# Kernel tuning notes

Hardware: AMD Instinct MI355X
Metric: run time of the kernel (lower is better)

Reference implementation:

```python
import jax, jax.numpy as jnp
import numpy as np
import itertools


def setup_inputs() -> dict:
    key = jax.random.key(0)
    k1, k2 = jax.random.split(key)
    vol = jax.random.normal(k1, (2, 160, 192, 224, 2), dtype=jnp.float32)
    trf = jax.random.normal(k2, (2, 160, 192, 224, 3), dtype=jnp.float32)
    return {"vol": vol, "trf": trf}


def _interpn_linear(vol, loc):
    """N-D multilinear interpolation of vol [*shape, C] at float locations.

    loc: list of ndims arrays, each [*shape], giving absolute sample coords.
    Out-of-domain points are clamped to the boundary (fill_value=None).
    Matches neurite's interpn('linear') math.
    """
    shape = vol.shape[:-1]
    ndims = len(shape)
    C = vol.shape[-1]
    maxs = [s - 1 for s in shape]

    # clip sample locations into the valid domain
    loc = [jnp.clip(l, 0.0, float(m)) for l, m in zip(loc, maxs)]
    loc0 = [jnp.clip(jnp.floor(l), 0.0, float(m)) for l, m in zip(loc, maxs)]
    loc1 = [jnp.clip(l0 + 1.0, 0.0, float(m)) for l0, m in zip(loc0, maxs)]
    # corner-0 weight is (loc1 - loc), corner-1 weight is its complement
    w_c0 = [l1 - l for l1, l in zip(loc1, loc)]
    w_c1 = [1.0 - w for w in w_c0]

    idx0 = [l.astype(jnp.int32) for l in loc0]
    idx1 = [l.astype(jnp.int32) for l in loc1]

    # row-major strides for flat gather
    strides = np.concatenate([np.cumprod(np.array(shape[::-1]))[::-1][1:], [1]]).astype(np.int32)
    vol_flat = vol.reshape(-1, C)

    out = jnp.zeros(shape + (C,), dtype=vol.dtype)
    for corner in itertools.product((0, 1), repeat=ndims):
        flat_idx = 0
        wt = 1.0
        for d in range(ndims):
            i = idx0[d] if corner[d] == 0 else idx1[d]
            w = w_c0[d] if corner[d] == 0 else w_c1[d]
            flat_idx = flat_idx + i * int(strides[d])
            wt = wt * w
        gathered = jnp.take(vol_flat, flat_idx, axis=0)  # [*shape, C]
        out = out + wt[..., None] * gathered
    return out


def reference(vol, trf):
    # single_transform=True: only the first batch element is used
    v = vol[0]   # [D1, D2, D3, C]
    t = trf[0]   # [D1, D2, D3, 3] dense shift (ij indexing)
    shape = v.shape[:-1]
    ndims = len(shape)
    # absolute sample locations = meshgrid + shift
    loc = []
    for d in range(ndims):
        ax = [1] * ndims
        ax[d] = shape[d]
        grid_d = jnp.arange(shape[d], dtype=t.dtype).reshape(ax)
        loc.append(grid_d + t[..., d])
    return _interpn_linear(v, loc)
```

## Files before the change

### kernel.cpp

```cpp
#include <hip/hip_runtime.h>


constexpr int D0 = 160, D1 = 192, D2 = 224;
constexpr int GT_K = D2 / 16;
constexpr int GT_J = D1 / 8;
constexpr int GT_I = D0 / 4;
constexpr int NBLOCKS = GT_K * GT_J * GT_I;

typedef float float4u __attribute__((ext_vector_type(4), aligned(8)));

__device__ __forceinline__ float2 sample_one(const float2* __restrict__ vol2,
                                             int i, int j, int k,
                                             float s0, float s1, float s2)
{
    float l0 = fminf(fmaxf((float)i + s0, 0.0f), (float)(D0 - 1));
    float l1 = fminf(fmaxf((float)j + s1, 0.0f), (float)(D1 - 1));
    float l2 = fminf(fmaxf((float)k + s2, 0.0f), (float)(D2 - 1));

    float f0 = floorf(l0), f1 = floorf(l1), f2 = floorf(l2);
    float g0 = fminf(f0 + 1.0f, (float)(D0 - 1));
    float g1 = fminf(f1 + 1.0f, (float)(D1 - 1));
    float g2 = fminf(f2 + 1.0f, (float)(D2 - 1));

    float w0a = g0 - l0, w1a = g1 - l1, w2a = g2 - l2;
    float w0b = 1.0f - w0a, w1b = 1.0f - w1a, w2b = 1.0f - w2a;

    int i0 = (int)f0, j0 = (int)f1, k0 = (int)f2;
    int i1 = (int)g0, j1 = (int)g1;
    int kb = min(k0, D2 - 2);

    int r0 = i0 * (D1 * D2), r1 = i1 * (D1 * D2);
    int c0 = j0 * D2,        c1 = j1 * D2;

    float4u q00 = *(const float4u*)(vol2 + (r0 + c0 + kb));
    float4u q01 = *(const float4u*)(vol2 + (r0 + c1 + kb));
    float4u q10 = *(const float4u*)(vol2 + (r1 + c0 + kb));
    float4u q11 = *(const float4u*)(vol2 + (r1 + c1 + kb));

    float v00x = w2a * q00.x + w2b * q00.z, v00y = w2a * q00.y + w2b * q00.w;
    float v01x = w2a * q01.x + w2b * q01.z, v01y = w2a * q01.y + w2b * q01.w;
    float v10x = w2a * q10.x + w2b * q10.z, v10y = w2a * q10.y + w2b * q10.w;
    float v11x = w2a * q11.x + w2b * q11.z, v11y = w2a * q11.y + w2b * q11.w;

    float waa = w0a * w1a, wab = w0a * w1b, wba = w0b * w1a, wbb = w0b * w1b;
    float2 r;
    r.x = waa * v00x + wab * v01x + wba * v10x + wbb * v11x;
    r.y = waa * v00y + wab * v01y + wba * v10y + wbb * v11y;
    return r;
}

__global__ __launch_bounds__(256) void st_trilinear4_kernel(
    const float* __restrict__ vol,
    const float* __restrict__ trf,
    float4* __restrict__ out)
{
    int b = blockIdx.x;
    int tk = b % GT_K;
    int tb = b / GT_K;
    int tj = tb % GT_J;
    int ti = tb / GT_J;

    int tid = threadIdx.x;
    int kp_l = tid & 7;
    int j_l  = (tid >> 3) & 7;
    int i_l  = tid >> 6;

    int i = ti * 4 + i_l;
    int j = tj * 8 + j_l;
    int k = (tk * 8 + kp_l) * 2;

    int v0 = (i * D1 + j) * D2 + k;
    int u = v0 >> 1;

    const float* tp = trf + 6 * (long long)u;
    float4u T0 = *(const float4u*)tp;
    float2  T1 = *(const float2*)(tp + 4);

    const float2* vol2 = (const float2*)vol;
    float2 A = sample_one(vol2, i, j, k,     T0.x, T0.y, T0.z);
    float2 B = sample_one(vol2, i, j, k + 1, T0.w, T1.x, T1.y);

    float4 o;
    o.x = A.x; o.y = A.y; o.z = B.x; o.w = B.y;
    out[u] = o;
}

extern "C" void kernel_launch(void* const* d_in, const int* in_sizes, int n_in,
                              void* d_out, int out_size, void* d_ws, size_t ws_size,
                              hipStream_t stream) {
    const float* vol = (const float*)d_in[0];
    const float* trf = (const float*)d_in[1];
    float4* out = (float4*)d_out;

    st_trilinear4_kernel<<<NBLOCKS, 256, 0, stream>>>(vol, trf, out);
}
```

Baseline: 301.1 us.

## Process four voxels per thread with nontemporal I/O and XCD-aware block swizzle

Each thread now computes four consecutive k voxels instead of two, loading its trf values as three aligned 16-byte vector loads and writing two 16-byte outputs. The trf loads and output stores are marked nontemporal so this streaming traffic is less likely to evict the cached volume. Block indices are remapped so that each group of eight consecutive hardware block IDs is spread across contiguous tile ranges, meant to keep neighbouring tiles on the same XCD and improve L2 reuse of volume gathers. In exchange, per-thread register use and gather count rise, and only half as many blocks are launched.

Result: slower. 330.0 us (+9.6%).

```diff
diff --git a/kernel.cpp b/kernel.cpp
--- a/kernel.cpp
+++ b/kernel.cpp
@@ -2,20 +2,23 @@
 
 
 constexpr int D0 = 160, D1 = 192, D2 = 224;
-constexpr int GT_K = D2 / 16;
-constexpr int GT_J = D1 / 8;
-constexpr int GT_I = D0 / 4;
-constexpr int NBLOCKS = GT_K * GT_J * GT_I;
+constexpr int TI = 8, TJ = 8, TK = 16;
+constexpr int GT_I = D0 / TI;
+constexpr int GT_J = D1 / TJ;
+constexpr int GT_K = D2 / TK;
+constexpr int NBLOCKS = GT_I * GT_J * GT_K;
+constexpr int CPX = NBLOCKS / 8;
 
 typedef float float4u __attribute__((ext_vector_type(4), aligned(8)));
+typedef float vfloat4 __attribute__((ext_vector_type(4)));
 
 __device__ __forceinline__ float2 sample_one(const float2* __restrict__ vol2,
-                                             int i, int j, int k,
+                                             float fi, float fj, float fk,
                                              float s0, float s1, float s2)
 {
-    float l0 = fminf(fmaxf((float)i + s0, 0.0f), (float)(D0 - 1));
-    float l1 = fminf(fmaxf((float)j + s1, 0.0f), (float)(D1 - 1));
-    float l2 = fminf(fmaxf((float)k + s2, 0.0f), (float)(D2 - 1));
+    float l0 = fminf(fmaxf(fi + s0, 0.0f), (float)(D0 - 1));
+    float l1 = fminf(fmaxf(fj + s1, 0.0f), (float)(D1 - 1));
+    float l2 = fminf(fmaxf(fk + s2, 0.0f), (float)(D2 - 1));
 
     float f0 = floorf(l0), f1 = floorf(l1), f2 = floorf(l2);
     float g0 = fminf(f0 + 1.0f, (float)(D0 - 1));
@@ -49,40 +52,48 @@
     return r;
 }
 
-__global__ __launch_bounds__(256) void st_trilinear4_kernel(
+__global__ __launch_bounds__(256) void st_trilinear8_kernel(
     const float* __restrict__ vol,
     const float* __restrict__ trf,
-    float4* __restrict__ out)
+    vfloat4* __restrict__ out)
 {
-    int b = blockIdx.x;
-    int tk = b % GT_K;
-    int tb = b / GT_K;
+    int b  = blockIdx.x;
+    int sw = (b & 7) * CPX + (b >> 3);
+
+    int tk = sw % GT_K;
+    int tb = sw / GT_K;
     int tj = tb % GT_J;
     int ti = tb / GT_J;
 
     int tid = threadIdx.x;
-    int kp_l = tid & 7;
-    int j_l  = (tid >> 3) & 7;
-    int i_l  = tid >> 6;
+    int kq  = tid & 3;
+    int j_l = (tid >> 2) & 7;
+    int i_l = tid >> 5;
 
-    int i = ti * 4 + i_l;
-    int j = tj * 8 + j_l;
-    int k = (tk * 8 + kp_l) * 2;
+    int i = ti * TI + i_l;
+    int j = tj * TJ + j_l;
+    int k = tk * TK + kq * 4;
 
     int v0 = (i * D1 + j) * D2 + k;
-    int u = v0 >> 1;
+    int u  = v0 >> 1;
 
-    const float* tp = trf + 6 * (long long)u;
-    float4u T0 = *(const float4u*)tp;
-    float2  T1 = *(const float2*)(tp + 4);
+    const float* tp = trf + 3 * (size_t)v0;
+    vfloat4 T0 = __builtin_nontemporal_load((const vfloat4*)tp);
+    vfloat4 T1 = __builtin_nontemporal_load((const vfloat4*)(tp + 4));
+    vfloat4 T2 = __builtin_nontemporal_load((const vfloat4*)(tp + 8));
 
     const float2* vol2 = (const float2*)vol;
-    float2 A = sample_one(vol2, i, j, k,     T0.x, T0.y, T0.z);
-    float2 B = sample_one(vol2, i, j, k + 1, T0.w, T1.x, T1.y);
+    float fi = (float)i, fj = (float)j, fk = (float)k;
 
-    float4 o;
-    o.x = A.x; o.y = A.y; o.z = B.x; o.w = B.y;
-    out[u] = o;
+    float2 A = sample_one(vol2, fi, fj, fk,        T0.x, T0.y, T0.z);
+    float2 B = sample_one(vol2, fi, fj, fk + 1.0f, T0.w, T1.x, T1.y);
+    float2 C = sample_one(vol2, fi, fj, fk + 2.0f, T1.z, T1.w, T2.x);
+    float2 D = sample_one(vol2, fi, fj, fk + 3.0f, T2.y, T2.z, T2.w);
+
+    vfloat4 o0 = { A.x, A.y, B.x, B.y };
+    vfloat4 o1 = { C.x, C.y, D.x, D.y };
+    __builtin_nontemporal_store(o0, &out[u]);
+    __builtin_nontemporal_store(o1, &out[u + 1]);
 }
 
 extern "C" void kernel_launch(void* const* d_in, const int* in_sizes, int n_in,
@@ -90,7 +101,7 @@
                               hipStream_t stream) {
     const float* vol = (const float*)d_in[0];
     const float* trf = (const float*)d_in[1];
-    float4* out = (float4*)d_out;
+    vfloat4* out = (vfloat4*)d_out;
 
-    st_trilinear4_kernel<<<NBLOCKS, 256, 0, stream>>>(vol, trf, out);
+    st_trilinear8_kernel<<<NBLOCKS, 256, 0, stream>>>(vol, trf, out);
 }
```
